# Kernel tuning notes

Measured on AMD Instinct MI355X. Metric: run time of the kernel, lower is better.

Reference implementation:

```python
import jax, jax.numpy as jnp
import numpy as np

SIGMA = 0.1
B_PARAM = 1.0
EPS_NORM = 1e-12  # torch F.normalize eps
EPS_MIN = 1e-5


def setup_inputs() -> dict:
    key = jax.random.key(0)
    k1, k2 = jax.random.split(key)
    x = jax.random.normal(k1, (4, 64, 64, 64), dtype=jnp.float32)
    y = jax.random.normal(k2, (4, 64, 64, 64), dtype=jnp.float32)
    return {"x": x, "y": y}


def reference(x, y):
    B, C, H, W = x.shape
    N = H * W
    xf = x.reshape(B, C, N)
    yf = y.reshape(B, C, N)
    # F.normalize along channel dim (L2, eps-clamped denominator)
    xn = xf / jnp.maximum(jnp.linalg.norm(xf, axis=1, keepdims=True), EPS_NORM)
    yn = yf / jnp.maximum(jnp.linalg.norm(yf, axis=1, keepdims=True), EPS_NORM)
    xt = jnp.transpose(xn, (0, 2, 1))  # [B, N, C]
    yt = jnp.transpose(yn, (0, 2, 1))  # [B, N, C]
    x2 = jnp.sum(xt * xt, axis=-1, keepdims=True)          # [B, N, 1]
    y2 = jnp.sum(yt * yt, axis=-1)[:, None, :]             # [B, 1, N]
    d2 = x2 + y2 - 2.0 * jnp.einsum('bnc,bmc->bnm', xt, yt)  # [B, N, N]
    dist = jnp.sqrt(jnp.maximum(d2, 0.0))
    d_min = jnp.min(dist, axis=-1, keepdims=True)
    d_scaled = dist / (d_min + EPS_MIN)
    w = jnp.exp((B_PARAM - d_scaled) / SIGMA)
    cx = w / jnp.sum(w, axis=-1, keepdims=True)
    cx_max = jnp.max(cx, axis=-1)  # [B, N]
    return -jnp.log(jnp.mean(cx_max + EPS_MIN))
```

## Files before the change

### kernel.cpp

```cpp
#include <hip/hip_runtime.h>
#include <math.h>

constexpr int B_   = 4;
constexpr int C_   = 64;
constexpr int HW   = 4096;
constexpr int ROWS = B_ * HW;

constexpr float SIGMA    = 0.1f;
constexpr float EPS_MIN  = 1e-5f;
constexpr float EPS_NORM = 1e-12f;
constexpr float LOG2E    = 1.44269504088896340736f;

constexpr int CC = 512;
constexpr int SR = 64;
constexpr int NS = CC / SR;
constexpr int XR = 128;

using short8  = __attribute__((ext_vector_type(8))) short;
using floatx4 = __attribute__((ext_vector_type(4))) float;

__device__ inline ushort f2bf(float f) {
    unsigned u = __float_as_uint(f);
    unsigned r = u + 0x7FFFu + ((u >> 16) & 1u);
    return (ushort)(r >> 16);
}

__global__ __launch_bounds__(256) void nrm_kernel(const float* __restrict__ x,
                                                  const float* __restrict__ y,
                                                  ushort* __restrict__ xn,
                                                  ushort* __restrict__ yn,
                                                  unsigned* __restrict__ dmin_u,
                                                  float* __restrict__ S) {
    int p = blockIdx.x * 256 + threadIdx.x;
    if (p < ROWS) { dmin_u[p] = 0x7F800000u; S[p] = 0.0f; }
    const float* src; ushort* dst; int q;
    if (p < ROWS) { src = x; dst = xn; q = p; }
    else          { src = y; dst = yn; q = p - ROWS; }
    int b = q >> 12;
    int n = q & (HW - 1);
    const float* base = src + ((size_t)b * C_) * HW + n;
    float v[C_];
    float ss = 0.0f;
#pragma unroll
    for (int c = 0; c < C_; ++c) {
        v[c] = base[(size_t)c * HW];
        ss = fmaf(v[c], v[c], ss);
    }
    float scale = 1.0f / fmaxf(sqrtf(ss), EPS_NORM);
    short8* o = (short8*)(dst + (size_t)q * C_);
#pragma unroll
    for (int c8 = 0; c8 < C_ / 8; ++c8) {
        short8 pk;
#pragma unroll
        for (int j = 0; j < 8; ++j) pk[j] = (short)f2bf(v[c8 * 8 + j] * scale);
        o[c8] = pk;
    }
}

template <int PASS>
__global__ __launch_bounds__(256, 4) void gemm_pass(const ushort* __restrict__ xn,
                                                    const ushort* __restrict__ yn,
                                                    unsigned* __restrict__ dmin_u,
                                                    float* __restrict__ S) {
    __shared__ short8 lds[2][SR * 8];

    int tid  = threadIdx.x;
    int wid  = tid >> 6;
    int lane = tid & 63;
    int lrow = lane & 15;
    int kblk = lane >> 4;

    int b     = blockIdx.z;
    int nbase = blockIdx.y * XR + wid * 32;
    int cbase = blockIdx.x * CC;

    const ushort* xb = xn + (size_t)(b * HW + nbase) * C_;
    const short8* yv = (const short8*)(yn + (size_t)(b * HW + cbase) * C_);

    short8 a0 = *(const short8*)(xb + lrow * C_ + kblk * 8);
    short8 a1 = *(const short8*)(xb + lrow * C_ + 32 + kblk * 8);
    short8 a2 = *(const short8*)(xb + (16 + lrow) * C_ + kblk * 8);
    short8 a3 = *(const short8*)(xb + (16 + lrow) * C_ + 32 + kblk * 8);

    int row0 = b * HW + nbase + kblk * 4;

    int wrow = tid >> 3, wslot = tid & 7;
    int w0 = wrow * 8 + (wslot ^ (wrow & 7));
    int w1 = (wrow + 32) * 8 + (wslot ^ (wrow & 7));

    float st[8];
    float kk2[8], c02[8];
    if (PASS == 0) {
#pragma unroll
        for (int r = 0; r < 8; ++r) st[r] = -INFINITY;
    } else {
#pragma unroll
        for (int r = 0; r < 8; ++r) {
            int row = row0 + (r >> 2) * 16 + (r & 3);
            float dm = __uint_as_float(dmin_u[row]);
            kk2[r] = LOG2E / (SIGMA * (dm + EPS_MIN));
            c02[r] = dm * kk2[r];
            st[r]  = 0.0f;
        }
    }

    {
        short8 v0 = yv[tid], v1 = yv[tid + 256];
        lds[0][w0] = v0;
        lds[0][w1] = v1;
    }
    __syncthreads();

    for (int s = 0; s < NS; ++s) {
        int cur = s & 1;
        short8 n0, n1;
        if (s + 1 < NS) {
            n0 = yv[(s + 1) * 512 + tid];
            n1 = yv[(s + 1) * 512 + 256 + tid];
        }
#pragma unroll
        for (int t4 = 0; t4 < 4; ++t4) {
            int r = t4 * 16 + lrow;
            int p = r & 7;
            short8 y0 = lds[cur][r * 8 + (kblk ^ p)];
            short8 y1 = lds[cur][r * 8 + ((kblk + 4) ^ p)];
            floatx4 acc0 = {0.0f, 0.0f, 0.0f, 0.0f};
            floatx4 acc1 = {0.0f, 0.0f, 0.0f, 0.0f};
            acc0 = __builtin_amdgcn_mfma_f32_16x16x32_bf16(a0, y0, acc0, 0, 0, 0);
            acc0 = __builtin_amdgcn_mfma_f32_16x16x32_bf16(a1, y1, acc0, 0, 0, 0);
            acc1 = __builtin_amdgcn_mfma_f32_16x16x32_bf16(a2, y0, acc1, 0, 0, 0);
            acc1 = __builtin_amdgcn_mfma_f32_16x16x32_bf16(a3, y1, acc1, 0, 0, 0);
#pragma unroll
            for (int r4 = 0; r4 < 8; ++r4) {
                float a = (r4 < 4) ? acc0[r4 & 3] : acc1[r4 & 3];
                if (PASS == 0) {
                    st[r4] = fmaxf(st[r4], a);
                } else {
                    float d2 = fmaxf(fmaf(-2.0f, a, 2.0f), 0.0f);
                    float d  = __builtin_amdgcn_sqrtf(d2);
                    st[r4] += __builtin_amdgcn_exp2f(fmaf(-kk2[r4], d, c02[r4]));
                }
            }
        }
        if (s + 1 < NS) {
            lds[cur ^ 1][w0] = n0;
            lds[cur ^ 1][w1] = n1;
        }
        __syncthreads();
    }

#pragma unroll
    for (int off = 1; off < 16; off <<= 1) {
#pragma unroll
        for (int r = 0; r < 8; ++r) {
            float o = __shfl_xor(st[r], off);
            st[r] = (PASS == 0) ? fmaxf(st[r], o) : (st[r] + o);
        }
    }
    if (lrow == 0) {
#pragma unroll
        for (int r = 0; r < 8; ++r) {
            int row = row0 + (r >> 2) * 16 + (r & 3);
            if (PASS == 0) {
                float d2 = fmaxf(fmaf(-2.0f, st[r], 2.0f), 0.0f);
                float d  = sqrtf(d2);
                atomicMin(&dmin_u[row], __float_as_uint(d));
            } else {
                atomicAdd(&S[row], st[r]);
            }
        }
    }
}

__global__ __launch_bounds__(256) void final_kernel(const float* __restrict__ S,
                                                    float* __restrict__ out) {
    const float4* S4 = (const float4*)S;
    float acc = 0.0f;
    for (int i = threadIdx.x; i < ROWS / 4; i += 256) {
        float4 v = S4[i];
        acc += __builtin_amdgcn_rcpf(v.x) + __builtin_amdgcn_rcpf(v.y) +
               __builtin_amdgcn_rcpf(v.z) + __builtin_amdgcn_rcpf(v.w) +
               4.0f * EPS_MIN;
    }
#pragma unroll
    for (int off = 32; off > 0; off >>= 1)
        acc += __shfl_down(acc, off);
    __shared__ float part[4];
    if ((threadIdx.x & 63) == 0) part[threadIdx.x >> 6] = acc;
    __syncthreads();
    if (threadIdx.x == 0) {
        float t = part[0] + part[1] + part[2] + part[3];
        out[0] = -logf(t / (float)ROWS);
    }
}

extern "C" void kernel_launch(void* const* d_in, const int* in_sizes, int n_in,
                              void* d_out, int out_size, void* d_ws, size_t ws_size,
                              hipStream_t stream) {
    const float* x = (const float*)d_in[0];
    const float* y = (const float*)d_in[1];
    float* out = (float*)d_out;

    char* ws = (char*)d_ws;
    size_t nrm_bytes = (size_t)ROWS * C_ * sizeof(ushort);
    ushort*   xn     = (ushort*)(ws);
    ushort*   yn     = (ushort*)(ws + nrm_bytes);
    unsigned* dmin_u = (unsigned*)(ws + 2 * nrm_bytes);
    float*    S      = (float*)(ws + 2 * nrm_bytes + (size_t)ROWS * sizeof(unsigned));

    hipLaunchKernelGGL(nrm_kernel, dim3(2 * ROWS / 256), dim3(256), 0, stream,
                       x, y, xn, yn, dmin_u, S);
    dim3 grid(HW / CC, HW / XR, B_);
    hipLaunchKernelGGL(gemm_pass<0>, grid, dim3(256), 0, stream,
                       xn, yn, dmin_u, S);
    hipLaunchKernelGGL(gemm_pass<1>, grid, dim3(256), 0, stream,
                       xn, yn, dmin_u, S);
    hipLaunchKernelGGL(final_kernel, dim3(1), dim3(256), 0, stream, S, out);
}
```

Baseline: 102.0 us.

## Swap MFMA operand roles and widen per-wave x tile to 64 rows

Each wave now holds 64 x rows in registers instead of 32, so every Y fragment read from LDS feeds four MFMA pairs instead of two. The MFMA operands are swapped so that x rows map to output columns. This makes the max and sum reductions in-register within each lane and leaves only a two-step cross-lane shuffle at the end. The cost is more registers per thread, so launch bounds drop from 4 to 2 blocks per SIMD, and the grid has half as many blocks along the row dimension.

```diff
diff --git a/kernel.cpp b/kernel.cpp
--- a/kernel.cpp
+++ b/kernel.cpp
@@ -14,7 +14,7 @@
 constexpr int CC = 512;
 constexpr int SR = 64;
 constexpr int NS = CC / SR;
-constexpr int XR = 128;
+constexpr int XR = 256;
 
 using short8  = __attribute__((ext_vector_type(8))) short;
 using floatx4 = __attribute__((ext_vector_type(4))) float;
@@ -58,7 +58,7 @@
 }
 
 template <int PASS>
-__global__ __launch_bounds__(256, 4) void gemm_pass(const ushort* __restrict__ xn,
+__global__ __launch_bounds__(256, 2) void gemm_pass(const ushort* __restrict__ xn,
                                                     const ushort* __restrict__ yn,
                                                     unsigned* __restrict__ dmin_u,
                                                     float* __restrict__ S) {
@@ -68,39 +68,40 @@
     int wid  = tid >> 6;
     int lane = tid & 63;
     int lrow = lane & 15;
-    int kblk = lane >> 4;
+    int kgrp = lane >> 4;
 
     int b     = blockIdx.z;
-    int nbase = blockIdx.y * XR + wid * 32;
+    int nbase = blockIdx.y * XR + wid * 64;
     int cbase = blockIdx.x * CC;
 
     const ushort* xb = xn + (size_t)(b * HW + nbase) * C_;
     const short8* yv = (const short8*)(yn + (size_t)(b * HW + cbase) * C_);
 
-    short8 a0 = *(const short8*)(xb + lrow * C_ + kblk * 8);
-    short8 a1 = *(const short8*)(xb + lrow * C_ + 32 + kblk * 8);
-    short8 a2 = *(const short8*)(xb + (16 + lrow) * C_ + kblk * 8);
-    short8 a3 = *(const short8*)(xb + (16 + lrow) * C_ + 32 + kblk * 8);
-
-    int row0 = b * HW + nbase + kblk * 4;
+    short8 xb0[4], xb1[4];
+#pragma unroll
+    for (int xt = 0; xt < 4; ++xt) {
+        xb0[xt] = *(const short8*)(xb + (xt * 16 + lrow) * C_ + kgrp * 8);
+        xb1[xt] = *(const short8*)(xb + (xt * 16 + lrow) * C_ + 32 + kgrp * 8);
+    }
+
+    int row0 = b * HW + nbase + lrow;
 
     int wrow = tid >> 3, wslot = tid & 7;
     int w0 = wrow * 8 + (wslot ^ (wrow & 7));
     int w1 = (wrow + 32) * 8 + (wslot ^ (wrow & 7));
 
-    float st[8];
-    float kk2[8], c02[8];
+    float st[4];
+    float kk2[4], c02[4];
     if (PASS == 0) {
 #pragma unroll
-        for (int r = 0; r < 8; ++r) st[r] = -INFINITY;
+        for (int xt = 0; xt < 4; ++xt) st[xt] = -INFINITY;
     } else {
 #pragma unroll
-        for (int r = 0; r < 8; ++r) {
-            int row = row0 + (r >> 2) * 16 + (r & 3);
-            float dm = __uint_as_float(dmin_u[row]);
-            kk2[r] = LOG2E / (SIGMA * (dm + EPS_MIN));
-            c02[r] = dm * kk2[r];
-            st[r]  = 0.0f;
+        for (int xt = 0; xt < 4; ++xt) {
+            float dm = __uint_as_float(dmin_u[row0 + xt * 16]);
+            kk2[xt] = LOG2E / (SIGMA * (dm + EPS_MIN));
+            c02[xt] = dm * kk2[xt];
+            st[xt]  = 0.0f;
         }
     }
 
@@ -119,26 +120,26 @@
             n1 = yv[(s + 1) * 512 + 256 + tid];
         }
 #pragma unroll
-        for (int t4 = 0; t4 < 4; ++t4) {
-            int r = t4 * 16 + lrow;
-            int p = r & 7;
-            short8 y0 = lds[cur][r * 8 + (kblk ^ p)];
-            short8 y1 = lds[cur][r * 8 + ((kblk + 4) ^ p)];
-            floatx4 acc0 = {0.0f, 0.0f, 0.0f, 0.0f};
-            floatx4 acc1 = {0.0f, 0.0f, 0.0f, 0.0f};
-            acc0 = __builtin_amdgcn_mfma_f32_16x16x32_bf16(a0, y0, acc0, 0, 0, 0);
-            acc0 = __builtin_amdgcn_mfma_f32_16x16x32_bf16(a1, y1, acc0, 0, 0, 0);
-            acc1 = __builtin_amdgcn_mfma_f32_16x16x32_bf16(a2, y0, acc1, 0, 0, 0);
-            acc1 = __builtin_amdgcn_mfma_f32_16x16x32_bf16(a3, y1, acc1, 0, 0, 0);
-#pragma unroll
-            for (int r4 = 0; r4 < 8; ++r4) {
-                float a = (r4 < 4) ? acc0[r4 & 3] : acc1[r4 & 3];
+        for (int yt = 0; yt < 4; ++yt) {
+            int p = yt * 16 + lrow;
+            int q = p & 7;
+            short8 ya0 = lds[cur][p * 8 + (kgrp ^ q)];
+            short8 ya1 = lds[cur][p * 8 + ((kgrp + 4) ^ q)];
+#pragma unroll
+            for (int xt = 0; xt < 4; ++xt) {
+                floatx4 acc = {0.0f, 0.0f, 0.0f, 0.0f};
+                acc = __builtin_amdgcn_mfma_f32_16x16x32_bf16(ya0, xb0[xt], acc, 0, 0, 0);
+                acc = __builtin_amdgcn_mfma_f32_16x16x32_bf16(ya1, xb1[xt], acc, 0, 0, 0);
                 if (PASS == 0) {
-                    st[r4] = fmaxf(st[r4], a);
+                    st[xt] = fmaxf(st[xt],
+                             fmaxf(fmaxf(acc[0], acc[1]), fmaxf(acc[2], acc[3])));
                 } else {
-                    float d2 = fmaxf(fmaf(-2.0f, a, 2.0f), 0.0f);
-                    float d  = __builtin_amdgcn_sqrtf(d2);
-                    st[r4] += __builtin_amdgcn_exp2f(fmaf(-kk2[r4], d, c02[r4]));
+#pragma unroll
+                    for (int r = 0; r < 4; ++r) {
+                        float d2 = fmaxf(fmaf(-2.0f, acc[r], 2.0f), 0.0f);
+                        float d  = __builtin_amdgcn_sqrtf(d2);
+                        st[xt] += __builtin_amdgcn_exp2f(fmaf(-kk2[xt], d, c02[xt]));
+                    }
                 }
             }
         }
@@ -150,23 +151,23 @@
     }
 
 #pragma unroll
-    for (int off = 1; off < 16; off <<= 1) {
-#pragma unroll
-        for (int r = 0; r < 8; ++r) {
-            float o = __shfl_xor(st[r], off);
-            st[r] = (PASS == 0) ? fmaxf(st[r], o) : (st[r] + o);
-        }
-    }
-    if (lrow == 0) {
-#pragma unroll
-        for (int r = 0; r < 8; ++r) {
-            int row = row0 + (r >> 2) * 16 + (r & 3);
+    for (int off = 16; off < 64; off <<= 1) {
+#pragma unroll
+        for (int xt = 0; xt < 4; ++xt) {
+            float o = __shfl_xor(st[xt], off);
+            st[xt] = (PASS == 0) ? fmaxf(st[xt], o) : (st[xt] + o);
+        }
+    }
+    if (kgrp == 0) {
+#pragma unroll
+        for (int xt = 0; xt < 4; ++xt) {
+            int row = row0 + xt * 16;
             if (PASS == 0) {
-                float d2 = fmaxf(fmaf(-2.0f, st[r], 2.0f), 0.0f);
+                float d2 = fmaxf(fmaf(-2.0f, st[xt], 2.0f), 0.0f);
                 float d  = sqrtf(d2);
                 atomicMin(&dmin_u[row], __float_as_uint(d));
             } else {
-                atomicAdd(&S[row], st[r]);
+                atomicAdd(&S[row], st[xt]);
             }
         }
     }
```

New measurement: 100.5 us. About the same (-1.4%).
